# Optimization experiments

Hardware: AMD Instinct MI355X
Metric: run time of the kernel (lower is better)

Reference implementation:

```python
import jax, jax.numpy as jnp
import numpy as np
import math

N_EMBD = 1024
N_HEAD_DIM = 64
B, S = 8, 2048

def setup_inputs() -> dict:
    key = jax.random.key(0)
    ks = jax.random.split(key, 8)
    x = jax.random.normal(ks[0], (B, S, N_EMBD), dtype=jnp.float32)
    padding_mask = jax.random.randint(ks[1], (B, S), 0, 2).astype(jnp.bool_)
    scale = 1.0 / math.sqrt(N_EMBD)
    Wq = jax.random.normal(ks[2], (N_HEAD_DIM, N_EMBD), dtype=jnp.float32) * scale
    bq = jnp.zeros((N_HEAD_DIM,), dtype=jnp.float32)
    Wk = jax.random.normal(ks[3], (N_HEAD_DIM, N_EMBD), dtype=jnp.float32) * scale
    bk = jnp.zeros((N_HEAD_DIM,), dtype=jnp.float32)
    Wv = jax.random.normal(ks[4], (N_HEAD_DIM, N_EMBD), dtype=jnp.float32) * scale
    bv = jnp.zeros((N_HEAD_DIM,), dtype=jnp.float32)
    return {"x": x, "Wq": Wq, "bq": bq, "Wk": Wk, "bk": bk, "Wv": Wv, "bv": bv,
            "padding_mask": padding_mask}

def reference(x, Wq, bq, Wk, bk, Wv, bv, padding_mask):
    # q,k,v: [B,S,D] via Linear (x @ W^T + b)
    q = jnp.einsum('bse,de->bsd', x, Wq) + bq
    k = jnp.einsum('bse,de->bsd', x, Wk) + bk
    v = jnp.einsum('bse,de->bsd', x, Wv) + bv
    scale = 1.0 / math.sqrt(k.shape[-1])
    att = jnp.einsum('bqd,bkd->bqk', q, k) * scale  # [B,S,S]
    # padding_mask [B,S] -> [B,1,S]: True positions masked to -inf
    att = jnp.where(padding_mask[:, None, :], -jnp.inf, att)
    att = jax.nn.softmax(att, axis=-1)
    # attn_dropout omitted (eval mode / identity)
    return jnp.einsum('bqk,bkd->bqd', att, v)
```

## Files before the change

kernel.cpp:

```cpp
#include <hip/hip_runtime.h>
#include <hip/hip_bf16.h>

#define B_ 8
#define S_ 2048
#define E_ 1024
#define D_ 64
#define VT_STRIDE 2112

typedef short short8 __attribute__((ext_vector_type(8)));
typedef short short4v __attribute__((ext_vector_type(4)));
typedef float floatx4 __attribute__((ext_vector_type(4)));

static __device__ __forceinline__ short bf16_bits(float f) {
    __hip_bfloat16 h = __float2bfloat16(f);
    return *reinterpret_cast<short*>(&h);
}
static __device__ __forceinline__ float bits_to_f(short s) {
    __hip_bfloat16 h = *reinterpret_cast<__hip_bfloat16*>(&s);
    return __bfloat162float(h);
}
static __device__ __forceinline__ void split8(const float* __restrict__ p,
                                              short8& hi, short8& lo) {
    #pragma unroll
    for (int j = 0; j < 8; j++) {
        float f = p[j];
        short h = bf16_bits(f);
        hi[j] = h;
        lo[j] = bf16_bits(f - bits_to_f(h));
    }
}
static __device__ __forceinline__ void split8v(const float v[8],
                                               short8& hi, short8& lo) {
    #pragma unroll
    for (int j = 0; j < 8; j++) {
        float f = v[j];
        short h = bf16_bits(f);
        hi[j] = h;
        lo[j] = bf16_bits(f - bits_to_f(h));
    }
}
static __device__ __forceinline__ void dma16(const void* src, void* lds_dst) {
    __builtin_amdgcn_global_load_lds(
        (const __attribute__((address_space(1))) unsigned int*)src,
        (__attribute__((address_space(3))) unsigned int*)lds_dst, 16, 0, 0);
}

__global__ __launch_bounds__(256) void prep_kernel(
    const float* __restrict__ Wq, const float* __restrict__ Wk,
    const float* __restrict__ Wv, short8* __restrict__ Wpk8,
    const void* __restrict__ mask_raw, float* __restrict__ maskf)
{
    __shared__ unsigned int red[256];
    if (blockIdx.x < 96) {
        const int t = blockIdx.x * 256 + threadIdx.x;
        const int l16  = t & 15;
        const int quad = (t >> 4) & 3;
        const int nb   = (t >> 6) & 3;
        const int m    = (t >> 8) % 3;
        const int e0c  = (t >> 8) / 3;
        const float* W = (m == 0) ? Wq : ((m == 1) ? Wk : Wv);
        short8 hi, lo;
        split8(W + (size_t)(nb * 16 + l16) * E_ + e0c * 32 + quad * 8, hi, lo);
        const size_t pos = (size_t)((e0c * 3 + m) * 2) * 256 + nb * 64 + quad * 16 + l16;
        Wpk8[pos]       = hi;
        Wpk8[pos + 256] = lo;
    } else {
        const unsigned int* w = (const unsigned int*)mask_raw;
        unsigned int local = 0;
        for (int i = threadIdx.x; i < 4096; i += 256) local |= w[i];
        red[threadIdx.x] = local;
        __syncthreads();
        for (int s = 128; s > 0; s >>= 1) {
            if (threadIdx.x < s) red[threadIdx.x] |= red[threadIdx.x + s];
            __syncthreads();
        }
        const unsigned int ov = red[0];
        const bool is_u8 = (ov > 1u) && ((ov >> 24) <= 1u);
        const int i = (blockIdx.x - 96) * 256 + threadIdx.x;
        int v;
        if (ov == 0u)      v = 0;
        else if (is_u8)    v = (int)((const unsigned char*)mask_raw)[i];
        else               v = (((const unsigned int*)mask_raw)[i] != 0u);
        maskf[i] = v ? -1e30f : 0.0f;
    }
}

__global__ __launch_bounds__(512, 4) void qkv_kernel(
    const float* __restrict__ x, const short8* __restrict__ Wpk8,
    const float* __restrict__ bq, const float* __restrict__ bk,
    const float* __restrict__ bv,
    short* __restrict__ Qhi, short* __restrict__ Qlo,
    short* __restrict__ Khi, short* __restrict__ Vt)
{
    __shared__ alignas(16) float  xs[2][1024];
    __shared__ alignas(16) short8 wt[2][1536];
    const int tid  = threadIdx.x;
    const int wave = tid >> 6;
    const int nb   = wave & 3;
    const int rt   = wave >> 2;
    const int lane = tid & 63;
    const int l16  = lane & 15;
    const int quad = lane >> 4;
    const int row0 = blockIdx.x * 32;

    const float* xsrc = x + (size_t)(row0 + (tid >> 3)) * E_ +
                        (((tid & 7) ^ ((tid >> 3) & 7)) * 4);

    floatx4 acc[3];
    #pragma unroll
    for (int m = 0; m < 3; m++) acc[m] = (floatx4){0.f,0.f,0.f,0.f};

    if (tid < 256) dma16(xsrc, &xs[0][tid * 4]);
    #pragma unroll
    for (int i = 0; i < 3; i++)
        dma16(Wpk8 + (size_t)i * 512 + tid, &wt[0][i * 512 + tid]);

    int buf = 0;
    for (int e0c = 0; e0c < 32; ++e0c) {
        __syncthreads();
        if (e0c + 1 < 32) {
            if (tid < 256) dma16(xsrc + (e0c + 1) * 32, &xs[buf ^ 1][tid * 4]);
            #pragma unroll
            for (int i = 0; i < 3; i++)
                dma16(Wpk8 + (size_t)(e0c + 1) * 1536 + i * 512 + tid,
                      &wt[buf ^ 1][i * 512 + tid]);
        }

        const int rr = rt * 16 + l16;
        const int rx = rr & 7;
        const float* xr = &xs[buf][rr * 32];
        float4 a0 = *reinterpret_cast<const float4*>(xr + (((2 * quad)     ^ rx) * 4));
        float4 a1 = *reinterpret_cast<const float4*>(xr + (((2 * quad + 1) ^ rx) * 4));
        float av[8] = {a0.x, a0.y, a0.z, a0.w, a1.x, a1.y, a1.z, a1.w};
        short8 ah, al;
        split8v(av, ah, al);

        #pragma unroll
        for (int m = 0; m < 3; m++) {
            short8 wh = wt[buf][(m * 2 + 0) * 256 + nb * 64 + lane];
            short8 wl = wt[buf][(m * 2 + 1) * 256 + nb * 64 + lane];
            acc[m] = __builtin_amdgcn_mfma_f32_16x16x32_bf16(al, wh, acc[m], 0, 0, 0);
            acc[m] = __builtin_amdgcn_mfma_f32_16x16x32_bf16(ah, wl, acc[m], 0, 0, 0);
            acc[m] = __builtin_amdgcn_mfma_f32_16x16x32_bf16(ah, wh, acc[m], 0, 0, 0);
        }
        buf ^= 1;
    }

    const int d = nb * 16 + l16;
    const float bqv = bq[d];
    const float bkv = bk[d];
    const float bvv = bv[d];
    const int bch = row0 >> 11;
    const int rowbase = row0 + rt * 16 + quad * 4;
    short4v vpk;
    #pragma unroll
    for (int r = 0; r < 4; r++) {
        const size_t row = (size_t)(rowbase + r);
        const float q = (acc[0][r] + bqv) * 0.125f;
        const short qhv = bf16_bits(q);
        Qhi[row * 64 + d] = qhv;
        Qlo[row * 64 + d] = bf16_bits(q - bits_to_f(qhv));
        Khi[row * 64 + d] = bf16_bits(acc[1][r] + bkv);
        vpk[r] = bf16_bits(acc[2][r] + bvv);
    }
    *reinterpret_cast<short4v*>(Vt + ((size_t)(bch * 64 + d)) * VT_STRIDE +
                                (rowbase & 2047)) = vpk;
}

union alignas(16) AttnLds {
    struct { short8 kts[4][512]; short8 vts[4][512]; } st;
    struct {
        float Osh[4][16][65];
        float msh[4][16], lsh[4][16];
    } mg;
};

__global__ __launch_bounds__(256, 2) void attn_kernel(
    const short* __restrict__ Qhi, const short* __restrict__ Qlo,
    const short* __restrict__ Khi, const short* __restrict__ Vt,
    const float* __restrict__ maskf, float* __restrict__ out)
{
    __shared__ AttnLds lds;
    __shared__ short PlT[4][16][72];

    const int tid  = threadIdx.x;
    const int wave = tid >> 6;
    const int qsub = wave & 1;
    const int par  = wave >> 1;
    const int lane = tid & 63;
    const int l16  = lane & 15;
    const int quad = lane >> 4;
    const int b    = blockIdx.x >> 6;
    const int qt   = blockIdx.x & 63;
    const size_t qbase  = (size_t)b * S_ + qt * 32 + qsub * 16;
    const size_t kplane = (size_t)b * S_;
    const short* Vb = Vt + (size_t)b * 64 * VT_STRIDE;

    short8 qh[2], ql[2];
    #pragma unroll
    for (int dc = 0; dc < 2; dc++) {
        qh[dc] = *reinterpret_cast<const short8*>(Qhi + (qbase + l16) * 64 + dc * 32 + quad * 8);
        ql[dc] = *reinterpret_cast<const short8*>(Qlo + (qbase + l16) * 64 + dc * 32 + quad * 8);
    }

    float m = -1e30f, l = 0.f;
    floatx4 O[4];
    #pragma unroll
    for (int ob = 0; ob < 4; ob++) O[ob] = (floatx4){0.f,0.f,0.f,0.f};

    #pragma unroll
    for (int p = 0; p < 2; p++) {
        #pragma unroll
        for (int i = 0; i < 2; i++) {
            const int c = i * 256 + tid;
            const int r = c >> 3, cs = c & 7;
            dma16(Khi + (kplane + p * 64 + r) * 64 + ((cs ^ (r & 7)) * 8),
                  &lds.st.kts[p][c]);
            dma16(Vb + (size_t)r * VT_STRIDE + p * 64 + ((cs ^ (r & 7)) * 8),
                  &lds.st.vts[p][c]);
        }
    }
    float4 mk4[4];
    #pragma unroll
    for (int kb = 0; kb < 4; kb++)
        mk4[kb] = *reinterpret_cast<const float4*>(
            maskf + kplane + par * 64 + kb * 16 + quad * 4);

    for (int R = 0; R < 16; ++R) {
        __syncthreads();
        const int set = R & 1;
        if (R + 1 < 16) {
            const int nset = set ^ 1;
            const int kt2 = (R + 1) * 128;
            #pragma unroll
            for (int p = 0; p < 2; p++) {
                #pragma unroll
                for (int i = 0; i < 2; i++) {
                    const int c = i * 256 + tid;
                    const int r = c >> 3, cs = c & 7;
                    dma16(Khi + (kplane + kt2 + p * 64 + r) * 64 + ((cs ^ (r & 7)) * 8),
                          &lds.st.kts[nset * 2 + p][c]);
                    dma16(Vb + (size_t)r * VT_STRIDE + kt2 + p * 64 + ((cs ^ (r & 7)) * 8),
                          &lds.st.vts[nset * 2 + p][c]);
                }
            }
        }
        const int buf = set * 2 + par;

        floatx4 sc[4];
        #pragma unroll
        for (int kb = 0; kb < 4; kb++) {
            floatx4 a = (floatx4){0.f,0.f,0.f,0.f};
            #pragma unroll
            for (int kc = 0; kc < 2; kc++) {
                const int key = kb * 16 + l16;
                short8 kf = lds.st.kts[buf][key * 8 + ((kc * 4 + quad) ^ (key & 7))];
                a = __builtin_amdgcn_mfma_f32_16x16x32_bf16(kf, qh[kc], a, 0, 0, 0);
                a = __builtin_amdgcn_mfma_f32_16x16x32_bf16(kf, ql[kc], a, 0, 0, 0);
            }
            sc[kb] = a;
        }
        #pragma unroll
        for (int kb = 0; kb < 4; kb++) {
            const float* mkp = reinterpret_cast<const float*>(&mk4[kb]);
            #pragma unroll
            for (int r = 0; r < 4; r++) sc[kb][r] += mkp[r];
        }

        if (R + 1 < 16) {
            const int ktn = (R + 1) * 128 + par * 64;
            #pragma unroll
            for (int kb = 0; kb < 4; kb++)
                mk4[kb] = *reinterpret_cast<const float4*>(
                    maskf + kplane + ktn + kb * 16 + quad * 4);
        }

        float mx = -1e30f;
        #pragma unroll
        for (int kb = 0; kb < 4; kb++)
            #pragma unroll
            for (int r = 0; r < 4; r++) mx = fmaxf(mx, sc[kb][r]);
        mx = fmaxf(mx, __shfl_xor(mx, 16, 64));
        mx = fmaxf(mx, __shfl_xor(mx, 32, 64));
        const float mnew  = fmaxf(fmaxf(m, mx), -1e29f);
        const float alpha = __expf(m - mnew);
        float ps = 0.f;
        #pragma unroll
        for (int kb = 0; kb < 4; kb++)
            #pragma unroll
            for (int r = 0; r < 4; r++) {
                const float pe = __expf(sc[kb][r] - mnew);
                sc[kb][r] = pe;
                ps += pe;
            }
        ps += __shfl_xor(ps, 16, 64);
        ps += __shfl_xor(ps, 32, 64);
        l = l * alpha + ps;
        m = mnew;
        #pragma unroll
        for (int ob = 0; ob < 4; ob++) O[ob] *= alpha;

        #pragma unroll
        for (int kb = 0; kb < 4; kb++)
            #pragma unroll
            for (int r = 0; r < 4; r++)
                PlT[wave][l16][kb * 16 + quad * 4 + r] = bf16_bits(sc[kb][r]);
        short8 pf[2];
        #pragma unroll
        for (int kc = 0; kc < 2; kc++)
            pf[kc] = *reinterpret_cast<const short8*>(&PlT[wave][l16][kc * 32 + quad * 8]);

        #pragma unroll
        for (int ob = 0; ob < 4; ob++)
            #pragma unroll
            for (int kc = 0; kc < 2; kc++) {
                const int dd = ob * 16 + l16;
                short8 vf = lds.st.vts[buf][dd * 8 + ((kc * 4 + quad) ^ (dd & 7))];
                O[ob] = __builtin_amdgcn_mfma_f32_16x16x32_bf16(vf, pf[kc], O[ob], 0, 0, 0);
            }
    }

    __syncthreads();
    #pragma unroll
    for (int ob = 0; ob < 4; ob++)
        #pragma unroll
        for (int r = 0; r < 4; r++)
            lds.mg.Osh[wave][l16][ob * 16 + quad * 4 + r] = O[ob][r];
    if (quad == 0) {
        lds.mg.msh[wave][l16] = m;
        lds.mg.lsh[wave][l16] = l;
    }
    __syncthreads();

    #pragma unroll
    for (int part = 0; part < 8; part++) {
        const int idx = part * 256 + tid;
        const int q = idx >> 6;
        const int d = idx & 63;
        const int w0 = (q >> 4), qq = q & 15;
        const float m0 = lds.mg.msh[w0][qq], m1 = lds.mg.msh[w0 + 2][qq];
        const float ms = fmaxf(m0, m1);
        const float x0 = __expf(m0 - ms), x1 = __expf(m1 - ms);
        const float lt = lds.mg.lsh[w0][qq] * x0 + lds.mg.lsh[w0 + 2][qq] * x1;
        const float oa = lds.mg.Osh[w0][qq][d] * x0 + lds.mg.Osh[w0 + 2][qq][d] * x1;
        out[((size_t)b * S_ + qt * 32 + q) * 64 + d] = oa / lt;
    }
}

extern "C" void kernel_launch(void* const* d_in, const int* in_sizes, int n_in,
                              void* d_out, int out_size, void* d_ws, size_t ws_size,
                              hipStream_t stream) {
    const float* x  = (const float*)d_in[0];
    const float* Wq = (const float*)d_in[1];
    const float* bq = (const float*)d_in[2];
    const float* Wk = (const float*)d_in[3];
    const float* bk = (const float*)d_in[4];
    const float* Wv = (const float*)d_in[5];
    const float* bv = (const float*)d_in[6];
    const void* mask = d_in[7];

    char* ws = (char*)d_ws;
    const size_t PLANE = (size_t)B_ * S_ * D_;
    short* Wpk = (short*)ws;
    short* Qhi = (short*)(ws + 768 * 1024);
    short* Qlo = Qhi + PLANE;
    short* Khi = Qlo + PLANE;
    short* Vt  = Khi + PLANE;
    float* maskf = (float*)(Vt + (size_t)512 * VT_STRIDE);

    prep_kernel<<<160, 256, 0, stream>>>(Wq, Wk, Wv, (short8*)Wpk, mask, maskf);
    qkv_kernel<<<512, 512, 0, stream>>>(x, (const short8*)Wpk, bq, bk, bv,
                                        Qhi, Qlo, Khi, Vt);
    attn_kernel<<<512, 256, 0, stream>>>(Qhi, Qlo, Khi, Vt, maskf,
                                         (float*)d_out);
}
```

Measured before the change: 168.1 us.

## Drop weight low-part split in QKV projection and double K-chunk per stage

The low-precision residual of the weights is no longer packed or multiplied, cutting the QKV projection from three to two MFMAs per tile and halving weight traffic. The freed shared memory is used to load two 32-wide E chunks per pipeline stage, which halves the loop iterations and barriers. This lowers accuracy of the projections, since the weights are now plain bf16 while x still gets hi/lo splitting.

```diff
diff --git a/kernel.cpp b/kernel.cpp
--- a/kernel.cpp
+++ b/kernel.cpp
@@ -61,9 +61,7 @@
         const float* W = (m == 0) ? Wq : ((m == 1) ? Wk : Wv);
         short8 hi, lo;
         split8(W + (size_t)(nb * 16 + l16) * E_ + e0c * 32 + quad * 8, hi, lo);
-        const size_t pos = (size_t)((e0c * 3 + m) * 2) * 256 + nb * 64 + quad * 16 + l16;
-        Wpk8[pos]       = hi;
-        Wpk8[pos + 256] = lo;
+        Wpk8[(size_t)e0c * 768 + m * 256 + nb * 64 + quad * 16 + l16] = hi;
     } else {
         const unsigned int* w = (const unsigned int*)mask_raw;
         unsigned int local = 0;
@@ -92,7 +90,7 @@
     short* __restrict__ Qhi, short* __restrict__ Qlo,
     short* __restrict__ Khi, short* __restrict__ Vt)
 {
-    __shared__ alignas(16) float  xs[2][1024];
+    __shared__ alignas(16) float  xs[2][2][1024];
     __shared__ alignas(16) short8 wt[2][1536];
     const int tid  = threadIdx.x;
     const int wave = tid >> 6;
@@ -103,45 +101,48 @@
     const int quad = lane >> 4;
     const int row0 = blockIdx.x * 32;
 
-    const float* xsrc = x + (size_t)(row0 + (tid >> 3)) * E_ +
-                        (((tid & 7) ^ ((tid >> 3) & 7)) * 4);
+    const int xr_  = (tid >> 3) & 31;
+    const int xc_  = tid >> 8;
+    const float* xsrc = x + (size_t)(row0 + xr_) * E_ + xc_ * 32 +
+                        (((tid & 7) ^ (xr_ & 7)) * 4);
+    const int xdst = xc_ * 1024 + xr_ * 32 + (tid & 7) * 4;
 
     floatx4 acc[3];
     #pragma unroll
     for (int m = 0; m < 3; m++) acc[m] = (floatx4){0.f,0.f,0.f,0.f};
 
-    if (tid < 256) dma16(xsrc, &xs[0][tid * 4]);
     #pragma unroll
     for (int i = 0; i < 3; i++)
         dma16(Wpk8 + (size_t)i * 512 + tid, &wt[0][i * 512 + tid]);
+    dma16(xsrc, &xs[0][0][0] + xdst);
 
     int buf = 0;
-    for (int e0c = 0; e0c < 32; ++e0c) {
+    for (int R = 0; R < 16; ++R) {
         __syncthreads();
-        if (e0c + 1 < 32) {
-            if (tid < 256) dma16(xsrc + (e0c + 1) * 32, &xs[buf ^ 1][tid * 4]);
+        if (R + 1 < 16) {
             #pragma unroll
             for (int i = 0; i < 3; i++)
-                dma16(Wpk8 + (size_t)(e0c + 1) * 1536 + i * 512 + tid,
+                dma16(Wpk8 + (size_t)(R + 1) * 1536 + i * 512 + tid,
                       &wt[buf ^ 1][i * 512 + tid]);
-        }
-
-        const int rr = rt * 16 + l16;
-        const int rx = rr & 7;
-        const float* xr = &xs[buf][rr * 32];
-        float4 a0 = *reinterpret_cast<const float4*>(xr + (((2 * quad)     ^ rx) * 4));
-        float4 a1 = *reinterpret_cast<const float4*>(xr + (((2 * quad + 1) ^ rx) * 4));
-        float av[8] = {a0.x, a0.y, a0.z, a0.w, a1.x, a1.y, a1.z, a1.w};
-        short8 ah, al;
-        split8v(av, ah, al);
-
-        #pragma unroll
-        for (int m = 0; m < 3; m++) {
-            short8 wh = wt[buf][(m * 2 + 0) * 256 + nb * 64 + lane];
-            short8 wl = wt[buf][(m * 2 + 1) * 256 + nb * 64 + lane];
-            acc[m] = __builtin_amdgcn_mfma_f32_16x16x32_bf16(al, wh, acc[m], 0, 0, 0);
-            acc[m] = __builtin_amdgcn_mfma_f32_16x16x32_bf16(ah, wl, acc[m], 0, 0, 0);
-            acc[m] = __builtin_amdgcn_mfma_f32_16x16x32_bf16(ah, wh, acc[m], 0, 0, 0);
+            dma16(xsrc + (R + 1) * 64, &xs[buf ^ 1][0][0] + xdst);
+        }
+
+        #pragma unroll
+        for (int c = 0; c < 2; c++) {
+            const int rr = rt * 16 + l16;
+            const int rx = rr & 7;
+            const float* xrp = &xs[buf][c][rr * 32];
+            float4 a0 = *reinterpret_cast<const float4*>(xrp + (((2 * quad)     ^ rx) * 4));
+            float4 a1 = *reinterpret_cast<const float4*>(xrp + (((2 * quad + 1) ^ rx) * 4));
+            float av[8] = {a0.x, a0.y, a0.z, a0.w, a1.x, a1.y, a1.z, a1.w};
+            short8 ah, al;
+            split8v(av, ah, al);
+            #pragma unroll
+            for (int m = 0; m < 3; m++) {
+                short8 wh = wt[buf][c * 768 + m * 256 + nb * 64 + lane];
+                acc[m] = __builtin_amdgcn_mfma_f32_16x16x32_bf16(al, wh, acc[m], 0, 0, 0);
+                acc[m] = __builtin_amdgcn_mfma_f32_16x16x32_bf16(ah, wh, acc[m], 0, 0, 0);
+            }
         }
         buf ^= 1;
     }
```

After: 154.8 us. 1.09x faster.
